# Kernel tuning notes

Measured on AMD Instinct MI355X. Metric: run time of the kernel, lower is better.

Reference implementation:

```python
import jax, jax.numpy as jnp
import numpy as np

N_HEAD = 16
N_QUERY_GROUPS = 4
HEAD_SIZE = 64
ROPE_THETA = 10000.0


def apply_rope(x, theta=ROPE_THETA):
    # x: (B, H, T, D) -- lucidrains interleaved-pair rotary embedding
    B, H, T, D = x.shape
    inv_freq = 1.0 / (theta ** (jnp.arange(0, D, 2, dtype=jnp.float32) / D))  # (D/2,)
    freqs = jnp.arange(T, dtype=jnp.float32)[:, None] * inv_freq[None, :]      # (T, D/2)
    freqs = jnp.repeat(freqs, 2, axis=-1)                                      # (T, D)
    cos = jnp.cos(freqs).astype(x.dtype)
    sin = jnp.sin(freqs).astype(x.dtype)
    x1 = x[..., 0::2]
    x2 = x[..., 1::2]
    rot = jnp.stack((-x2, x1), axis=-1).reshape(x.shape)  # rotate_half, interleaved
    return x * cos + rot * sin


def setup_inputs() -> dict:
    key = jax.random.key(0)
    k1, k2, k3 = jax.random.split(key, 3)
    n_embd = N_HEAD * HEAD_SIZE
    qkv_dim = (N_HEAD + 2 * N_QUERY_GROUPS) * HEAD_SIZE
    x = jax.random.normal(k1, (1, 2048, n_embd), dtype=jnp.float32)
    w_attn = jax.random.normal(k2, (n_embd, qkv_dim), dtype=jnp.float32) * (n_embd ** -0.5)
    w_proj = jax.random.normal(k3, (n_embd, n_embd), dtype=jnp.float32) * (n_embd ** -0.5)
    return {"x": x, "w_attn": w_attn, "w_proj": w_proj}


def reference(x, w_attn, w_proj):
    B, T, C = x.shape
    q_per_kv = N_HEAD // N_QUERY_GROUPS
    total_qkv = q_per_kv + 2
    qkv = (x @ w_attn).reshape(B, T, N_QUERY_GROUPS, total_qkv, HEAD_SIZE)
    q = qkv[:, :, :, :q_per_kv, :].reshape(B, T, N_HEAD, HEAD_SIZE)
    k = qkv[:, :, :, q_per_kv:q_per_kv + 1, :].reshape(B, T, N_QUERY_GROUPS, HEAD_SIZE)
    v = qkv[:, :, :, q_per_kv + 1:, :].reshape(B, T, N_QUERY_GROUPS, HEAD_SIZE)
    # (B, H, T, D)
    q = q.transpose(0, 2, 1, 3)
    k = k.transpose(0, 2, 1, 3)
    v = v.transpose(0, 2, 1, 3)
    q = apply_rope(q)
    k = apply_rope(k)
    # GQA: broadcast each kv group to its q_per_kv query heads (repeat_interleave)
    k = jnp.repeat(k, q_per_kv, axis=1)
    v = jnp.repeat(v, q_per_kv, axis=1)
    scale = 1.0 / jnp.sqrt(jnp.asarray(HEAD_SIZE, dtype=q.dtype))
    att = jnp.einsum('bhqd,bhkd->bhqk', q, k) * scale
    causal = jnp.tril(jnp.ones((T, T), dtype=bool))
    att = jnp.where(causal, att, jnp.asarray(-jnp.inf, dtype=att.dtype))
    att = jax.nn.softmax(att, axis=-1)
    y = jnp.einsum('bhqk,bhkd->bhqd', att, v)
    y = y.transpose(0, 2, 1, 3).reshape(B, T, N_HEAD * HEAD_SIZE)
    return y @ w_proj
```

## Files before the change

kernel.cpp:

```cpp
#include <hip/hip_runtime.h>

#define T_SEQ 2048
#define C_EMB 1024
#define C_QKV 1536
#define N_HEAD 16

typedef __bf16 bf16x8 __attribute__((ext_vector_type(8)));
typedef __bf16 bf16x4 __attribute__((ext_vector_type(4)));
typedef float  f32x4  __attribute__((ext_vector_type(4)));

__device__ __forceinline__ void load_lds16(const __bf16* g, __bf16* l)
{
    __builtin_amdgcn_global_load_lds(
        (const __attribute__((address_space(1))) unsigned int*)g,
        (__attribute__((address_space(3))) unsigned int*)l, 16, 0, 0);
}

__device__ __forceinline__ void tconv_tile(
    const float* __restrict__ in, __bf16* __restrict__ out,
    int R, int C, int r0, int c0, float (*lds)[65], int t)
{
#pragma unroll
    for (int k = 0; k < 16; k++) {
        int r = k * 4 + (t >> 6), c = t & 63;
        lds[r][c] = in[(size_t)(r0 + r) * C + c0 + c];
    }
    __syncthreads();
#pragma unroll
    for (int k = 0; k < 16; k++) {
        int cc = k * 4 + (t >> 6), rr = t & 63;
        out[(size_t)(c0 + cc) * R + r0 + rr] = (__bf16)lds[rr][cc];
    }
}

__global__ __launch_bounds__(256) void prep_kernel(
    const float* __restrict__ x, const float* __restrict__ wa,
    const float* __restrict__ wp, __bf16* __restrict__ x_bf,
    __bf16* __restrict__ waT, __bf16* __restrict__ wpT)
{
    __shared__ float lds[64][65];
    const int b = blockIdx.x, t = threadIdx.x;
    if (b < 384) {
        tconv_tile(wa, waT, C_EMB, C_QKV, (b / 24) * 64, (b % 24) * 64, lds, t);
    } else if (b < 640) {
        int b2 = b - 384;
        tconv_tile(wp, wpT, C_EMB, C_EMB, (b2 / 16) * 64, (b2 % 16) * 64, lds, t);
    } else {
        for (int gi = (b - 640) * 256 + t; gi < T_SEQ * C_EMB / 8; gi += 65536) {
            float4 v0 = ((const float4*)x)[gi * 2];
            float4 v1 = ((const float4*)x)[gi * 2 + 1];
            bf16x8 o = { (__bf16)v0.x, (__bf16)v0.y, (__bf16)v0.z, (__bf16)v0.w,
                         (__bf16)v1.x, (__bf16)v1.y, (__bf16)v1.z, (__bf16)v1.w };
            ((bf16x8*)x_bf)[gi] = o;
        }
    }
}

template <bool FUSE_QKV>
__global__ __launch_bounds__(256) void gemm_mfma_kernel(
    const __bf16* __restrict__ A, const __bf16* __restrict__ Bt,
    __bf16* __restrict__ Cq, __bf16* __restrict__ Vt,
    float* __restrict__ Cf, int M, int N, int K)
{
    __shared__ __align__(16) __bf16 As0[64 * 64], As1[64 * 64];
    __shared__ __align__(16) __bf16 Bs0[64 * 64], Bs1[64 * 64];

    const int tid = threadIdx.x;
    const int l = tid & 63, w = tid >> 6;
    const int ln = l & 15, q = l >> 4;
    const int wm = (w & 1) * 32, wn = (w >> 1) * 32;
    const int row0 = blockIdx.y * 64, col0 = blockIdx.x * 64;

    f32x4 acc[2][2];
#pragma unroll
    for (int mi = 0; mi < 2; mi++)
#pragma unroll
        for (int ni = 0; ni < 2; ni++) acc[mi][ni] = (f32x4){0.f, 0.f, 0.f, 0.f};

    auto stage = [&](int k0, __bf16* as, __bf16* bs) {
#pragma unroll
        for (int p = 0; p < 2; p++) {
            int r = p * 32 + w * 8 + (l >> 3);
            int cc = (l & 7) ^ (r & 7);
            load_lds16(A + (size_t)(row0 + r) * K + k0 + cc * 8,
                       as + p * 2048 + w * 512);
            load_lds16(Bt + (size_t)(col0 + r) * K + k0 + cc * 8,
                       bs + p * 2048 + w * 512);
        }
    };
    auto compute = [&](const __bf16* as, const __bf16* bs) {
#pragma unroll
        for (int ki = 0; ki < 2; ki++) {
            bf16x8 af[2], bfr[2];
#pragma unroll
            for (int mi = 0; mi < 2; mi++)
                af[mi] = *(const bf16x8*)&as[(wm + mi * 16 + ln) * 64 +
                                             (((ki * 4 + q) ^ (ln & 7)) * 8)];
#pragma unroll
            for (int ni = 0; ni < 2; ni++)
                bfr[ni] = *(const bf16x8*)&bs[(wn + ni * 16 + ln) * 64 +
                                              (((ki * 4 + q) ^ (ln & 7)) * 8)];
#pragma unroll
            for (int mi = 0; mi < 2; mi++)
#pragma unroll
                for (int ni = 0; ni < 2; ni++)
                    acc[mi][ni] = __builtin_amdgcn_mfma_f32_16x16x32_bf16(
                        af[mi], bfr[ni], acc[mi][ni], 0, 0, 0);
        }
    };

    stage(0, As0, Bs0);
    for (int k0 = 0;; k0 += 128) {
        __syncthreads();
        if (k0 + 64 < K) stage(k0 + 64, As1, Bs1);
        compute(As0, Bs0);
        if (k0 + 64 >= K) break;
        __syncthreads();
        if (k0 + 128 < K) stage(k0 + 128, As0, Bs0);
        compute(As1, Bs1);
        if (k0 + 128 >= K) break;
    }

#pragma unroll
    for (int mi = 0; mi < 2; mi++)
#pragma unroll
        for (int ni = 0; ni < 2; ni++) {
            const int col = col0 + wn + ni * 16 + ln;
            if (!FUSE_QKV) {
#pragma unroll
                for (int reg = 0; reg < 4; reg++) {
                    int row = row0 + wm + mi * 16 + 4 * q + reg;
                    Cf[(size_t)row * N + col] = acc[mi][ni][reg];
                }
            } else {
                const int r = col % 384;
                const int gg = col / 384;
                if (r < 320) {
                    const int d = r & 63;
                    const float inv_freq =
                        __expf(-(float)(d & ~1) * (9.210340371976184f / 64.0f));
                    const float sgn = (d & 1) ? 1.0f : -1.0f;
                    const float osc = (r < 256) ? 0.18033688011112042f : 1.0f;
#pragma unroll
                    for (int reg = 0; reg < 4; reg++) {
                        int row = row0 + wm + mi * 16 + 4 * q + reg;
                        float v = acc[mi][ni][reg];
                        float pv = __shfl_xor(v, 1, 64);
                        float sn, cs;
                        sincosf((float)row * inv_freq, &sn, &cs);
                        Cq[(size_t)row * C_QKV + col] =
                            (__bf16)((v * cs + sgn * pv * sn) * osc);
                    }
                } else {
                    const int d = r - 320;
#pragma unroll
                    for (int reg = 0; reg < 4; reg++) {
                        int row = row0 + wm + mi * 16 + 4 * q + reg;
                        Vt[(size_t)(gg * 64 + d) * T_SEQ + row] =
                            (__bf16)acc[mi][ni][reg];
                    }
                }
            }
        }
}

__global__ __launch_bounds__(256) void attn_mfma_kernel(
    const __bf16* __restrict__ qkv, const __bf16* __restrict__ Vt,
    __bf16* __restrict__ y, __bf16* __restrict__ Opart,
    float* __restrict__ lpart)
{
    __shared__ __align__(16) __bf16 Ks0[64 * 64], Ks1[64 * 64];
    __shared__ __align__(16) __bf16 Vs0[64 * 64], Vs1[64 * 64];
    __shared__ __align__(16) __bf16 Ps[64 * 72];

    const int tid = threadIdx.x;
    const int l = tid & 63, w = tid >> 6;
    const int ln = l & 15, q = l >> 4;
    const int x = blockIdx.x, h = blockIdx.y;
    int qb, t0, t1;
    bool partial;
    if (x < 16)      { qb = 15 - x;  t0 = 0;             t1 = qb + 1;        partial = false; }
    else if (x < 32) { qb = x;       t0 = 0;             t1 = (qb + 2) >> 1; partial = true;  }
    else             { qb = x - 16;  t0 = (qb + 2) >> 1; t1 = qb + 1;        partial = true;  }

    const int g = h >> 2, hj = h & 3;
    const int qbase = g * 384 + hj * 64;
    const int kbase = g * 384 + 256;

    const int qrow = qb * 64 + w * 16 + ln;
    bf16x8 qa[2];
#pragma unroll
    for (int ki = 0; ki < 2; ki++)
        qa[ki] = *(const bf16x8*)(qkv + (size_t)qrow * C_QKV + qbase +
                                  ki * 32 + q * 8);

    f32x4 O[4];
#pragma unroll
    for (int ni = 0; ni < 4; ni++) O[ni] = (f32x4){0.f, 0.f, 0.f, 0.f};
    float lsum = 0.f;

    auto stage = [&](int kt, __bf16* ks, __bf16* vs) {
#pragma unroll
        for (int p = 0; p < 2; p++) {
            int r = p * 32 + w * 8 + (l >> 3);
            int cc = (l & 7) ^ (r & 7);
            load_lds16(qkv + (size_t)(kt * 64 + r) * C_QKV + kbase + cc * 8,
                       ks + p * 2048 + w * 512);
            load_lds16(Vt + (size_t)(g * 64 + r) * T_SEQ + kt * 64 + cc * 8,
                       vs + p * 2048 + w * 512);
        }
    };
    auto compute = [&](int kt, const __bf16* ks, const __bf16* vs) {
        f32x4 s[4];
#pragma unroll
        for (int ni = 0; ni < 4; ni++) s[ni] = (f32x4){0.f, 0.f, 0.f, 0.f};
#pragma unroll
        for (int ki = 0; ki < 2; ki++)
#pragma unroll
            for (int ni = 0; ni < 4; ni++) {
                bf16x8 kb = *(const bf16x8*)&ks[(ni * 16 + ln) * 64 +
                                                (((ki * 4 + q) ^ (ln & 7)) * 8)];
                s[ni] = __builtin_amdgcn_mfma_f32_16x16x32_bf16(
                    kb, qa[ki], s[ni], 0, 0, 0);
            }

        const bool diag = (kt == qb);
#pragma unroll
        for (int ni = 0; ni < 4; ni++) {
            bf16x4 pp;
#pragma unroll
            for (int reg = 0; reg < 4; reg++) {
                float v = s[ni][reg];
                if (diag && (ni * 16 + 4 * q + reg) > (w * 16 + ln)) v = -1e30f;
                float p = exp2f(v);
                lsum += p;
                pp[reg] = (__bf16)p;
            }
            *(bf16x4*)&Ps[(w * 16 + ln) * 72 + ni * 16 + 4 * q] = pp;
        }

#pragma unroll
        for (int ki = 0; ki < 2; ki++) {
            bf16x8 pa = *(const bf16x8*)&Ps[(w * 16 + ln) * 72 +
                                            ki * 32 + q * 8];
#pragma unroll
            for (int ni = 0; ni < 4; ni++) {
                bf16x8 vb = *(const bf16x8*)&vs[(ni * 16 + ln) * 64 +
                                                (((ki * 4 + q) ^ (ln & 7)) * 8)];
                O[ni] = __builtin_amdgcn_mfma_f32_16x16x32_bf16(
                    vb, pa, O[ni], 0, 0, 0);
            }
        }
    };

    stage(t0, Ks0, Vs0);
    for (int kt = t0;;) {
        __syncthreads();
        if (kt + 1 < t1) stage(kt + 1, Ks1, Vs1);
        compute(kt, Ks0, Vs0);
        if (++kt >= t1) break;
        __syncthreads();
        if (kt + 1 < t1) stage(kt + 1, Ks0, Vs0);
        compute(kt, Ks1, Vs1);
        if (++kt >= t1) break;
    }

    float ls = lsum;
    ls += __shfl_xor(ls, 16, 64);
    ls += __shfl_xor(ls, 32, 64);
    const int t = qb * 64 + w * 16 + ln;

    if (!partial) {
        const float inv = 1.0f / ls;
#pragma unroll
        for (int ni = 0; ni < 4; ni++) {
            bf16x4 o;
#pragma unroll
            for (int reg = 0; reg < 4; reg++) o[reg] = (__bf16)(O[ni][reg] * inv);
            *(bf16x4*)&y[(size_t)t * C_EMB + h * 64 + ni * 16 + 4 * q] = o;
        }
    } else {
        const int half = (x >= 32);
        const int tr = t - 1024;
        __bf16* od = Opart + (size_t)half * 1024 * C_EMB +
                     (size_t)tr * C_EMB + h * 64;
        if (q == 0) lpart[half * 16 * 1024 + h * 1024 + tr] = ls;
#pragma unroll
        for (int ni = 0; ni < 4; ni++) {
            bf16x4 o;
#pragma unroll
            for (int reg = 0; reg < 4; reg++) o[reg] = (__bf16)O[ni][reg];
            *(bf16x4*)&od[ni * 16 + 4 * q] = o;
        }
    }
}

__global__ __launch_bounds__(256) void merge_kernel(
    const __bf16* __restrict__ Opart, const float* __restrict__ lpart,
    __bf16* __restrict__ y)
{
    const size_t base = ((size_t)blockIdx.x * 256 + threadIdx.x) * 8;
    const int tr = (int)(base >> 10);
    const int c = (int)(base & 1023);
    const int h = c >> 6;
    const float inv = 1.0f / (lpart[h * 1024 + tr] +
                              lpart[16 * 1024 + h * 1024 + tr]);
    bf16x8 a = *(const bf16x8*)&Opart[base];
    bf16x8 b = *(const bf16x8*)&Opart[(size_t)1024 * C_EMB + base];
    bf16x8 o;
#pragma unroll
    for (int i = 0; i < 8; i++)
        o[i] = (__bf16)(((float)a[i] + (float)b[i]) * inv);
    *(bf16x8*)&y[(size_t)(1024 + tr) * C_EMB + c] = o;
}

extern "C" void kernel_launch(void* const* d_in, const int* in_sizes, int n_in,
                              void* d_out, int out_size, void* d_ws, size_t ws_size,
                              hipStream_t stream)
{
    const float* x      = (const float*)d_in[0];
    const float* w_attn = (const float*)d_in[1];
    const float* w_proj = (const float*)d_in[2];
    float* out = (float*)d_out;

    __bf16* x_bf = (__bf16*)d_ws;
    __bf16* waT  = x_bf + (size_t)T_SEQ * C_EMB;
    __bf16* wpT  = waT  + (size_t)C_QKV * C_EMB;
    __bf16* qkv  = wpT  + (size_t)C_EMB * C_EMB;
    __bf16* Vt   = qkv  + (size_t)T_SEQ * C_QKV;
    __bf16* y_bf = Vt   + (size_t)256 * T_SEQ;
    __bf16* Opart = x_bf;
    float*  lpart = (float*)waT;

    prep_kernel<<<896, 256, 0, stream>>>(x, w_attn, w_proj, x_bf, waT, wpT);

    gemm_mfma_kernel<true><<<dim3(C_QKV / 64, T_SEQ / 64), 256, 0, stream>>>(
        x_bf, waT, qkv, Vt, nullptr, T_SEQ, C_QKV, C_EMB);

    attn_mfma_kernel<<<dim3(48, N_HEAD), 256, 0, stream>>>(
        qkv, Vt, y_bf, Opart, lpart);

    merge_kernel<<<512, 256, 0, stream>>>(Opart, lpart, y_bf);

    gemm_mfma_kernel<false><<<dim3(C_EMB / 64, T_SEQ / 64), 256, 0, stream>>>(
        y_bf, wpT, nullptr, nullptr, out, T_SEQ, C_EMB, C_EMB);
}
```

Baseline: 119.5 us.

## Use two waves per attention block, each handling 32 query rows

The attention kernel now launches 128 threads per block instead of 256. Each wave processes two 16-row query sub-tiles, so every K and V fragment read from LDS feeds two MFMAs. The staging loop is reshaped so two waves still fill the same 64x64 K/V tiles. This cuts LDS read traffic per MFMA, but per-wave register use roughly doubles and each block has fewer waves to hide latency.

```diff
diff --git a/kernel.cpp b/kernel.cpp
--- a/kernel.cpp
+++ b/kernel.cpp
@@ -164,7 +164,7 @@
         }
 }
 
-__global__ __launch_bounds__(256) void attn_mfma_kernel(
+__global__ __launch_bounds__(128) void attn_mfma_kernel(
     const __bf16* __restrict__ qkv, const __bf16* __restrict__ Vt,
     __bf16* __restrict__ y, __bf16* __restrict__ Opart,
     float* __restrict__ lpart)
@@ -187,68 +187,85 @@
     const int qbase = g * 384 + hj * 64;
     const int kbase = g * 384 + 256;
 
-    const int qrow = qb * 64 + w * 16 + ln;
-    bf16x8 qa[2];
-#pragma unroll
-    for (int ki = 0; ki < 2; ki++)
-        qa[ki] = *(const bf16x8*)(qkv + (size_t)qrow * C_QKV + qbase +
-                                  ki * 32 + q * 8);
-
-    f32x4 O[4];
-#pragma unroll
-    for (int ni = 0; ni < 4; ni++) O[ni] = (f32x4){0.f, 0.f, 0.f, 0.f};
-    float lsum = 0.f;
+    bf16x8 qa[2][2];
+#pragma unroll
+    for (int qj = 0; qj < 2; qj++) {
+        const int qrow = qb * 64 + w * 32 + qj * 16 + ln;
+#pragma unroll
+        for (int ki = 0; ki < 2; ki++)
+            qa[qj][ki] = *(const bf16x8*)(qkv + (size_t)qrow * C_QKV + qbase +
+                                          ki * 32 + q * 8);
+    }
+
+    f32x4 O[2][4];
+#pragma unroll
+    for (int qj = 0; qj < 2; qj++)
+#pragma unroll
+        for (int ni = 0; ni < 4; ni++) O[qj][ni] = (f32x4){0.f, 0.f, 0.f, 0.f};
+    float lsum[2] = {0.f, 0.f};
 
     auto stage = [&](int kt, __bf16* ks, __bf16* vs) {
 #pragma unroll
-        for (int p = 0; p < 2; p++) {
-            int r = p * 32 + w * 8 + (l >> 3);
+        for (int p = 0; p < 4; p++) {
+            int r = p * 16 + w * 8 + (l >> 3);
             int cc = (l & 7) ^ (r & 7);
             load_lds16(qkv + (size_t)(kt * 64 + r) * C_QKV + kbase + cc * 8,
-                       ks + p * 2048 + w * 512);
+                       ks + p * 1024 + w * 512);
             load_lds16(Vt + (size_t)(g * 64 + r) * T_SEQ + kt * 64 + cc * 8,
-                       vs + p * 2048 + w * 512);
+                       vs + p * 1024 + w * 512);
         }
     };
     auto compute = [&](int kt, const __bf16* ks, const __bf16* vs) {
-        f32x4 s[4];
-#pragma unroll
-        for (int ni = 0; ni < 4; ni++) s[ni] = (f32x4){0.f, 0.f, 0.f, 0.f};
+        f32x4 s[2][4];
+#pragma unroll
+        for (int qj = 0; qj < 2; qj++)
+#pragma unroll
+            for (int ni = 0; ni < 4; ni++) s[qj][ni] = (f32x4){0.f, 0.f, 0.f, 0.f};
 #pragma unroll
         for (int ki = 0; ki < 2; ki++)
 #pragma unroll
             for (int ni = 0; ni < 4; ni++) {
                 bf16x8 kb = *(const bf16x8*)&ks[(ni * 16 + ln) * 64 +
                                                 (((ki * 4 + q) ^ (ln & 7)) * 8)];
-                s[ni] = __builtin_amdgcn_mfma_f32_16x16x32_bf16(
-                    kb, qa[ki], s[ni], 0, 0, 0);
+#pragma unroll
+                for (int qj = 0; qj < 2; qj++)
+                    s[qj][ni] = __builtin_amdgcn_mfma_f32_16x16x32_bf16(
+                        kb, qa[qj][ki], s[qj][ni], 0, 0, 0);
             }
 
         const bool diag = (kt == qb);
 #pragma unroll
-        for (int ni = 0; ni < 4; ni++) {
-            bf16x4 pp;
-#pragma unroll
-            for (int reg = 0; reg < 4; reg++) {
-                float v = s[ni][reg];
-                if (diag && (ni * 16 + 4 * q + reg) > (w * 16 + ln)) v = -1e30f;
-                float p = exp2f(v);
-                lsum += p;
-                pp[reg] = (__bf16)p;
-            }
-            *(bf16x4*)&Ps[(w * 16 + ln) * 72 + ni * 16 + 4 * q] = pp;
-        }
+        for (int qj = 0; qj < 2; qj++)
+#pragma unroll
+            for (int ni = 0; ni < 4; ni++) {
+                bf16x4 pp;
+#pragma unroll
+                for (int reg = 0; reg < 4; reg++) {
+                    float v = s[qj][ni][reg];
+                    if (diag && (ni * 16 + 4 * q + reg) > (w * 32 + qj * 16 + ln))
+                        v = -1e30f;
+                    float p = exp2f(v);
+                    lsum[qj] += p;
+                    pp[reg] = (__bf16)p;
+                }
+                *(bf16x4*)&Ps[(w * 32 + qj * 16 + ln) * 72 + ni * 16 + 4 * q] = pp;
+            }
 
 #pragma unroll
         for (int ki = 0; ki < 2; ki++) {
-            bf16x8 pa = *(const bf16x8*)&Ps[(w * 16 + ln) * 72 +
-                                            ki * 32 + q * 8];
+            bf16x8 pa[2];
+#pragma unroll
+            for (int qj = 0; qj < 2; qj++)
+                pa[qj] = *(const bf16x8*)&Ps[(w * 32 + qj * 16 + ln) * 72 +
+                                             ki * 32 + q * 8];
 #pragma unroll
             for (int ni = 0; ni < 4; ni++) {
                 bf16x8 vb = *(const bf16x8*)&vs[(ni * 16 + ln) * 64 +
                                                 (((ki * 4 + q) ^ (ln & 7)) * 8)];
-                O[ni] = __builtin_amdgcn_mfma_f32_16x16x32_bf16(
-                    vb, pa, O[ni], 0, 0, 0);
+#pragma unroll
+                for (int qj = 0; qj < 2; qj++)
+                    O[qj][ni] = __builtin_amdgcn_mfma_f32_16x16x32_bf16(
+                        vb, pa[qj], O[qj][ni], 0, 0, 0);
             }
         }
     };
@@ -265,32 +282,35 @@
         if (++kt >= t1) break;
     }
 
-    float ls = lsum;
-    ls += __shfl_xor(ls, 16, 64);
-    ls += __shfl_xor(ls, 32, 64);
-    const int t = qb * 64 + w * 16 + ln;
-
-    if (!partial) {
-        const float inv = 1.0f / ls;
-#pragma unroll
-        for (int ni = 0; ni < 4; ni++) {
-            bf16x4 o;
-#pragma unroll
-            for (int reg = 0; reg < 4; reg++) o[reg] = (__bf16)(O[ni][reg] * inv);
-            *(bf16x4*)&y[(size_t)t * C_EMB + h * 64 + ni * 16 + 4 * q] = o;
-        }
-    } else {
-        const int half = (x >= 32);
-        const int tr = t - 1024;
-        __bf16* od = Opart + (size_t)half * 1024 * C_EMB +
-                     (size_t)tr * C_EMB + h * 64;
-        if (q == 0) lpart[half * 16 * 1024 + h * 1024 + tr] = ls;
-#pragma unroll
-        for (int ni = 0; ni < 4; ni++) {
-            bf16x4 o;
-#pragma unroll
-            for (int reg = 0; reg < 4; reg++) o[reg] = (__bf16)O[ni][reg];
-            *(bf16x4*)&od[ni * 16 + 4 * q] = o;
+#pragma unroll
+    for (int qj = 0; qj < 2; qj++) {
+        float ls = lsum[qj];
+        ls += __shfl_xor(ls, 16, 64);
+        ls += __shfl_xor(ls, 32, 64);
+        const int t = qb * 64 + w * 32 + qj * 16 + ln;
+
+        if (!partial) {
+            const float inv = 1.0f / ls;
+#pragma unroll
+            for (int ni = 0; ni < 4; ni++) {
+                bf16x4 o;
+#pragma unroll
+                for (int reg = 0; reg < 4; reg++) o[reg] = (__bf16)(O[qj][ni][reg] * inv);
+                *(bf16x4*)&y[(size_t)t * C_EMB + h * 64 + ni * 16 + 4 * q] = o;
+            }
+        } else {
+            const int half = (x >= 32);
+            const int tr = t - 1024;
+            __bf16* od = Opart + (size_t)half * 1024 * C_EMB +
+                         (size_t)tr * C_EMB + h * 64;
+            if (q == 0) lpart[half * 16 * 1024 + h * 1024 + tr] = ls;
+#pragma unroll
+            for (int ni = 0; ni < 4; ni++) {
+                bf16x4 o;
+#pragma unroll
+                for (int reg = 0; reg < 4; reg++) o[reg] = (__bf16)O[qj][ni][reg];
+                *(bf16x4*)&od[ni * 16 + 4 * q] = o;
+            }
         }
     }
 }
@@ -337,7 +357,7 @@
     gemm_mfma_kernel<true><<<dim3(C_QKV / 64, T_SEQ / 64), 256, 0, stream>>>(
         x_bf, waT, qkv, Vt, nullptr, T_SEQ, C_QKV, C_EMB);
 
-    attn_mfma_kernel<<<dim3(48, N_HEAD), 256, 0, stream>>>(
+    attn_mfma_kernel<<<dim3(48, N_HEAD), 128, 0, stream>>>(
         qkv, Vt, y_bf, Opart, lpart);
 
     merge_kernel<<<512, 256, 0, stream>>>(Opart, lpart, y_bf);
```

Result: slower. 129.2 us (+8.1%).

## Read K and V tiles directly from global memory instead of LDS double-buffering

Applied to the files above, without the earlier changes.

Drops the LDS double-buffered staging of K and V tiles, which used async global-to-LDS loads and block-wide barriers. Each wave now loads its MFMA K and V operands straight from global memory through the cache. This removes the barriers and the LDS traffic, but every wave re-reads the same K/V tiles (four waves per block) and loses the prefetch overlap, which puts more load on L2 and adds latency. The Ps scratch stays in LDS and is still written and read per wave with no barrier.

```diff
diff --git a/kernel.cpp b/kernel.cpp
--- a/kernel.cpp
+++ b/kernel.cpp
@@ -169,8 +169,6 @@
     __bf16* __restrict__ y, __bf16* __restrict__ Opart,
     float* __restrict__ lpart)
 {
-    __shared__ __align__(16) __bf16 Ks0[64 * 64], Ks1[64 * 64];
-    __shared__ __align__(16) __bf16 Vs0[64 * 64], Vs1[64 * 64];
     __shared__ __align__(16) __bf16 Ps[64 * 72];
 
     const int tid = threadIdx.x;
@@ -194,23 +192,15 @@
         qa[ki] = *(const bf16x8*)(qkv + (size_t)qrow * C_QKV + qbase +
                                   ki * 32 + q * 8);
 
+    const __bf16* Kb = qkv + kbase;
+    const __bf16* Vb = Vt + (size_t)g * 64 * T_SEQ;
+
     f32x4 O[4];
 #pragma unroll
     for (int ni = 0; ni < 4; ni++) O[ni] = (f32x4){0.f, 0.f, 0.f, 0.f};
     float lsum = 0.f;
 
-    auto stage = [&](int kt, __bf16* ks, __bf16* vs) {
-#pragma unroll
-        for (int p = 0; p < 2; p++) {
-            int r = p * 32 + w * 8 + (l >> 3);
-            int cc = (l & 7) ^ (r & 7);
-            load_lds16(qkv + (size_t)(kt * 64 + r) * C_QKV + kbase + cc * 8,
-                       ks + p * 2048 + w * 512);
-            load_lds16(Vt + (size_t)(g * 64 + r) * T_SEQ + kt * 64 + cc * 8,
-                       vs + p * 2048 + w * 512);
-        }
-    };
-    auto compute = [&](int kt, const __bf16* ks, const __bf16* vs) {
+    for (int kt = t0; kt < t1; ++kt) {
         f32x4 s[4];
 #pragma unroll
         for (int ni = 0; ni < 4; ni++) s[ni] = (f32x4){0.f, 0.f, 0.f, 0.f};
@@ -218,8 +208,9 @@
         for (int ki = 0; ki < 2; ki++)
 #pragma unroll
             for (int ni = 0; ni < 4; ni++) {
-                bf16x8 kb = *(const bf16x8*)&ks[(ni * 16 + ln) * 64 +
-                                                (((ki * 4 + q) ^ (ln & 7)) * 8)];
+                bf16x8 kb = *(const bf16x8*)&Kb[
+                    (size_t)(kt * 64 + ni * 16 + ln) * C_QKV +
+                    (ki * 4 + q) * 8];
                 s[ni] = __builtin_amdgcn_mfma_f32_16x16x32_bf16(
                     kb, qa[ki], s[ni], 0, 0, 0);
             }
@@ -245,24 +236,13 @@
                                             ki * 32 + q * 8];
 #pragma unroll
             for (int ni = 0; ni < 4; ni++) {
-                bf16x8 vb = *(const bf16x8*)&vs[(ni * 16 + ln) * 64 +
-                                                (((ki * 4 + q) ^ (ln & 7)) * 8)];
+                bf16x8 vb = *(const bf16x8*)&Vb[
+                    (size_t)(ni * 16 + ln) * T_SEQ + kt * 64 +
+                    (ki * 4 + q) * 8];
                 O[ni] = __builtin_amdgcn_mfma_f32_16x16x32_bf16(
                     vb, pa, O[ni], 0, 0, 0);
             }
         }
-    };
-
-    stage(t0, Ks0, Vs0);
-    for (int kt = t0;;) {
-        __syncthreads();
-        if (kt + 1 < t1) stage(kt + 1, Ks1, Vs1);
-        compute(kt, Ks0, Vs0);
-        if (++kt >= t1) break;
-        __syncthreads();
-        if (kt + 1 < t1) stage(kt + 1, Ks0, Vs0);
-        compute(kt, Ks1, Vs1);
-        if (++kt >= t1) break;
     }
 
     float ls = lsum;
```

After: 170.6 us. 42.7% more time.
